# Kernel tuning notes

Hardware: AMD Instinct MI355X
Metric: run time of the kernel (lower is better)

## Reference

```python
import jax, jax.numpy as jnp
import numpy as np
from jax import lax

NUM_HEADS = 1
DN = ('NCHW', 'OIHW', 'NCHW')
EPS = 1e-12  # F.normalize default eps


def _l2_normalize(t):
    # F.normalize(t, dim=-1): t / max(||t||_2, eps)
    n = jnp.sqrt(jnp.sum(t * t, axis=-1, keepdims=True))
    return t / jnp.maximum(n, EPS)


def setup_inputs() -> dict:
    key = jax.random.key(0)
    k0, k1, k2, k3 = jax.random.split(key, 4)
    b, c, h, w = 4, 48, 256, 256
    x = jax.random.normal(k0, (b, c, h, w), dtype=jnp.float32)
    qkv_w = jax.random.normal(k1, (3 * c, c, 1, 1), dtype=jnp.float32) * 0.05
    dw_w = jax.random.normal(k2, (3 * c, 1, 3, 3), dtype=jnp.float32) * 0.05
    proj_w = jax.random.normal(k3, (c, c, 1, 1), dtype=jnp.float32) * 0.05
    temperature = jnp.ones((NUM_HEADS, 1, 1), dtype=jnp.float32)
    return {"x": x, "qkv_w": qkv_w, "dw_w": dw_w, "proj_w": proj_w,
            "temperature": temperature}


def reference(x, qkv_w, dw_w, proj_w, temperature):
    b, c, h, w = x.shape
    heads = NUM_HEADS
    # 1x1 conv to 3c channels, then 3x3 depthwise conv (groups = 3c)
    qkv = lax.conv_general_dilated(x, qkv_w, (1, 1), 'VALID', dimension_numbers=DN)
    qkv = lax.conv_general_dilated(qkv, dw_w, (1, 1), ((1, 1), (1, 1)),
                                   feature_group_count=3 * c, dimension_numbers=DN)
    q, k, v = jnp.split(qkv, 3, axis=1)
    # [b, heads, c_per_head, h*w]
    q = q.reshape(b, heads, c // heads, h * w)
    k = k.reshape(b, heads, c // heads, h * w)
    v = v.reshape(b, heads, c // heads, h * w)
    q = _l2_normalize(q)
    k = _l2_normalize(k)
    # channel-wise attention: [b, heads, c_per_head, c_per_head]
    attn = jax.nn.softmax(jnp.einsum('bhcn,bhdn->bhcd', q, k) * temperature, axis=-1)
    out = jnp.einsum('bhcd,bhdn->bhcn', attn, v).reshape(b, c, h, w)
    return lax.conv_general_dilated(out, proj_w, (1, 1), 'VALID', dimension_numbers=DN)
```

## Files before the change

### kernel.cpp

```cpp
#include <hip/hip_runtime.h>

#define B 4
#define C 48
#define C3 144
#define H 256
#define W 256
#define HW 65536
#define EPSN 1e-12f

#define TSX 16
#define TSY 12
#define HSX 18
#define HSY 14
#define NTX 16
#define NTY 22
#define NPIX2 192
#define NHALO 252

#define NCHUNK 128
#define CHUNK 512
#define LP 68

#define S_QKV_OFF  ((size_t)0)
#define S_DWQ_OFF  (S_QKV_OFF + (size_t)B * C3 * HW)
#define S_DWK_OFF  (S_DWQ_OFF + (size_t)B * C * HW)
#define S_SP_OFF   (S_DWK_OFF + (size_t)B * C * HW)
#define S_NQP_OFF  (S_SP_OFF + (size_t)B * NCHUNK * C * C)
#define S_NKP_OFF  (S_NQP_OFF + (size_t)B * NCHUNK * C)
#define S_S_OFF    (S_NKP_OFF + (size_t)B * NCHUNK * C)
#define S_NQ_OFF   (S_S_OFF + (size_t)B * C * C)
#define S_NK_OFF   (S_NQ_OFF + (size_t)B * C)
#define S_M_OFF    (S_NK_OFF + (size_t)B * C)
#define S_WT_OFF   (S_M_OFF + (size_t)B * C * C)
#define S_FLOATS   (S_WT_OFF + (size_t)C3 * C)

#define A_DWQ_OFF  ((size_t)0)
#define A_DWK_OFF  (A_DWQ_OFF + (size_t)B * C * HW)
#define A_SP_OFF   (A_DWK_OFF + (size_t)B * C * HW)
#define A_NQP_OFF  (A_SP_OFF + (size_t)B * NCHUNK * C * C)
#define A_NKP_OFF  (A_NQP_OFF + (size_t)B * NCHUNK * C)
#define A_S_OFF    (A_NKP_OFF + (size_t)B * NCHUNK * C)
#define A_NQ_OFF   (A_S_OFF + (size_t)B * C * C)
#define A_NK_OFF   (A_NQ_OFF + (size_t)B * C)
#define A_M_OFF    (A_NK_OFF + (size_t)B * C)
#define A_FLOATS   (A_M_OFF + (size_t)B * C * C)

#define B_S_OFF  0
#define B_NQ_OFF (B * C * C)
#define B_NK_OFF (B_NQ_OFF + B * C)
#define B_M_OFF  (B_NK_OFF + B * C)
#define B_ZERO_N (B * C * C + 2 * B * C)


__global__ __launch_bounds__(256) void s_wt(
    const float* __restrict__ w1, float* __restrict__ wT) {
  const int i = blockIdx.x * 256 + threadIdx.x;
  if (i < C3 * C) {
    const int oc = i / C, d = i - oc * C;
    wT[d * C3 + oc] = w1[i];
  }
}

__global__ __launch_bounds__(256) void s_conv1x1(
    const float* __restrict__ x, const float* __restrict__ wT,
    float* __restrict__ qkv) {
  __shared__ float xs[C * 256];
  const int t = threadIdx.x;
  const int bb = blockIdx.x >> 8;
  const int p0 = (blockIdx.x & 255) << 8;
  const float* xb = x + (size_t)bb * C * HW + p0;
#pragma unroll
  for (int j = 0; j < 12; ++j) {
    const int f = t + j * 256;
    const int d = f >> 6, p4 = (f & 63) * 4;
    *(float4*)&xs[d * 256 + p4] = *(const float4*)&xb[(size_t)d * HW + p4];
  }
  __syncthreads();
  const int pl = (t & 63) * 4;
  const int ocw = __builtin_amdgcn_readfirstlane((t >> 6) * 12);
#pragma unroll 1
  for (int g = 0; g < 3; ++g) {
    const int oc0 = g * 48 + ocw;
    const float* wp = wT + oc0;
    float acc[12][4];
#pragma unroll
    for (int o = 0; o < 12; ++o)
#pragma unroll
      for (int p = 0; p < 4; ++p) acc[o][p] = 0.f;
#pragma unroll 4
    for (int d = 0; d < C; ++d) {
      const float4 xv = *(const float4*)&xs[d * 256 + pl];
      const float xa[4] = {xv.x, xv.y, xv.z, xv.w};
#pragma unroll
      for (int jj = 0; jj < 3; ++jj) {
        const float4 wv = *(const float4*)&wp[d * C3 + jj * 4];
        const float wa[4] = {wv.x, wv.y, wv.z, wv.w};
#pragma unroll
        for (int o = 0; o < 4; ++o)
#pragma unroll
          for (int p = 0; p < 4; ++p)
            acc[jj * 4 + o][p] = fmaf(wa[o], xa[p], acc[jj * 4 + o][p]);
      }
    }
    float* ob = qkv + ((size_t)bb * C3 + oc0) * HW + p0 + pl;
#pragma unroll
    for (int o = 0; o < 12; ++o) {
      float4 v;
      v.x = acc[o][0]; v.y = acc[o][1]; v.z = acc[o][2]; v.w = acc[o][3];
      *(float4*)&ob[(size_t)o * HW] = v;
    }
  }
}

#define DWR 16
__global__ __launch_bounds__(256) void s_dw(
    const float* __restrict__ qkv, const float* __restrict__ w9,
    float* __restrict__ dwq, float* __restrict__ dwk,
    float* __restrict__ vout) {
  __shared__ float ls[18 * 260];
  const int t = threadIdx.x;
  const int rblk = blockIdx.x & 15;
  const int cb = blockIdx.x >> 4;
  const int c = cb % C3;
  const int bb = cb / C3;
  const int r0 = rblk * DWR;
  const float* src = qkv + (size_t)cb * HW;
#pragma unroll
  for (int f = t; f < 18 * 256; f += 256) {
    const int rr = f >> 8, xc = f & 255;
    const int gr = r0 - 1 + rr;
    ls[rr * 260 + 1 + xc] = (gr >= 0 && gr < H) ? src[gr * W + xc] : 0.f;
  }
  if (t < 18) { ls[t * 260] = 0.f; ls[t * 260 + 257] = 0.f; }
  const float* wp = w9 + c * 9;
  float wv[9];
#pragma unroll
  for (int k = 0; k < 9; ++k) wv[k] = wp[k];
  __syncthreads();
  float* dst;
  int cc;
  if (c < C)          { dst = dwq;  cc = c; }
  else if (c < 2 * C) { dst = dwk;  cc = c - C; }
  else                { dst = vout; cc = c - 2 * C; }
  float* ob = dst + ((size_t)bb * C + cc) * HW;
  const int xx = t;
#pragma unroll
  for (int ry = 0; ry < DWR; ++ry) {
    const float* l0 = ls + ry * 260 + xx;
    float d = wv[0] * l0[0] + wv[1] * l0[1] + wv[2] * l0[2];
    d = fmaf(wv[3], l0[260], d);
    d = fmaf(wv[4], l0[261], d);
    d = fmaf(wv[5], l0[262], d);
    d = fmaf(wv[6], l0[520], d);
    d = fmaf(wv[7], l0[521], d);
    d = fmaf(wv[8], l0[522], d);
    ob[(r0 + ry) * W + xx] = d;
  }
}


__global__ __launch_bounds__(256) void a1_conv_dw(
    const float* __restrict__ x, const float* __restrict__ w1,
    const float* __restrict__ w9, float* __restrict__ dwq,
    float* __restrict__ dwk, float* __restrict__ vout) {
  __shared__ float xs[C * 256];
  __shared__ float qs[8 * 256];
  __shared__ float wg[C * 8];
  __shared__ float wg9[8 * 9];
  const int t = threadIdx.x;
  const int bb = blockIdx.x / (NTX * NTY);
  const int tile = blockIdx.x % (NTX * NTY);
  const int ty = tile / NTX, tx = tile % NTX;

  const int hyy = t / HSX, hxx = t % HSX;
  const int hy = ty * TSY - 1 + hyy;
  const int hx = tx * TSX - 1 + hxx;
  const bool hin = (t < NHALO) && (hy >= 0) && (hy < H) && (hx >= 0) && (hx < W);
  const float* xb = x + (size_t)bb * C * HW + (hin ? (hy * W + hx) : 0);
#pragma unroll
  for (int ic = 0; ic < C; ++ic)
    xs[ic * 256 + t] = hin ? xb[(size_t)ic * HW] : 0.f;

  const int py = t / TSX, px = t % TSX;
  const int gy = ty * TSY + py, gx = tx * TSX + px;
  const bool pin = (t < NPIX2) && (gy < H);
  const int hpos = py * HSX + px;

  for (int grp = 0; grp < 18; ++grp) {
    const int ch0 = grp * 8;
    {
      const int j = t + ((t < 128) ? 256 : 0);
      if (t < 128) {
        const int ic = t >> 3, g = t & 7;
        wg[t] = w1[(ch0 + g) * C + ic];
        const int ic2 = j >> 3, g2 = j & 7;
        wg[j] = w1[(ch0 + g2) * C + ic2];
      } else if (t < 256) {
        const int r = t - 128;
        const int ic = (r + 128) >> 3, g = (r + 128) & 7;
        wg[r + 128] = w1[(ch0 + g) * C + ic];
      }
      if (t < 72) wg9[t] = w9[ch0 * 9 + t];
    }
    __syncthreads();

    float a[8];
#pragma unroll
    for (int g = 0; g < 8; ++g) a[g] = 0.f;
#pragma unroll 4
    for (int ic = 0; ic < C; ++ic) {
      const float xsv = xs[ic * 256 + t];
      const float4 w0 = *(const float4*)&wg[ic * 8];
      const float4 w4 = *(const float4*)&wg[ic * 8 + 4];
      a[0] = fmaf(w0.x, xsv, a[0]);
      a[1] = fmaf(w0.y, xsv, a[1]);
      a[2] = fmaf(w0.z, xsv, a[2]);
      a[3] = fmaf(w0.w, xsv, a[3]);
      a[4] = fmaf(w4.x, xsv, a[4]);
      a[5] = fmaf(w4.y, xsv, a[5]);
      a[6] = fmaf(w4.z, xsv, a[6]);
      a[7] = fmaf(w4.w, xsv, a[7]);
    }
#pragma unroll
    for (int g = 0; g < 8; ++g) qs[g * 256 + t] = a[g];
    __syncthreads();
    if (t < NPIX2) {
#pragma unroll
      for (int g = 0; g < 8; ++g) {
        const int ch = ch0 + g;
        const float* w9p = wg9 + g * 9;
        const float* q = qs + g * 256 + hpos;
        float d = w9p[0] * q[0] + w9p[1] * q[1] + w9p[2] * q[2];
        d = fmaf(w9p[3], q[HSX], d);
        d = fmaf(w9p[4], q[HSX + 1], d);
        d = fmaf(w9p[5], q[HSX + 2], d);
        d = fmaf(w9p[6], q[2 * HSX], d);
        d = fmaf(w9p[7], q[2 * HSX + 1], d);
        d = fmaf(w9p[8], q[2 * HSX + 2], d);
        if (pin) {
          float* dst;
          int cc;
          if (ch < C)          { dst = dwq; cc = ch; }
          else if (ch < 2 * C) { dst = dwk; cc = ch - C; }
          else                 { dst = vout; cc = ch - 2 * C; }
          dst[((size_t)bb * C + cc) * HW + gy * W + gx] = d;
        }
      }
    }
    __syncthreads();
  }
}

__global__ __launch_bounds__(256) void a2_gram(
    const float* __restrict__ dwq, const float* __restrict__ dwk,
    float* __restrict__ Sp, float* __restrict__ nqp, float* __restrict__ nkp) {
  __shared__ float qs[C * LP];
  __shared__ float ks[C * LP];
  const int tid = threadIdx.x;
  const int bb = blockIdx.x / NCHUNK;
  const int chunk = blockIdx.x % NCHUNK;
  const int base = chunk * CHUNK;
  const float* qb = dwq + (size_t)bb * C * HW + base;
  const float* kb = dwk + (size_t)bb * C * HW + base;
  const int c0 = (tid >> 4) * 3;
  const int d0 = (tid & 15) * 3;
  float acc[3][3] = {{0.f}};
  float nacc = 0.f;
  for (int sub = 0; sub < CHUNK / 64; ++sub) {
    __syncthreads();
#pragma unroll
    for (int j = 0; j < 3; ++j) {
      const int f = tid + j * 256;
      const int cc = f >> 4, p4 = (f & 15) * 4;
      *(float4*)&qs[cc * LP + p4] = *(const float4*)&qb[(size_t)cc * HW + sub * 64 + p4];
      *(float4*)&ks[cc * LP + p4] = *(const float4*)&kb[(size_t)cc * HW + sub * 64 + p4];
    }
    __syncthreads();
    if (tid < C) {
#pragma unroll
      for (int pp = 0; pp < 64; ++pp) { const float v = qs[tid * LP + pp]; nacc = fmaf(v, v, nacc); }
    } else if (tid >= 64 && tid < 64 + C) {
      const int c = tid - 64;
#pragma unroll
      for (int pp = 0; pp < 64; ++pp) { const float v = ks[c * LP + pp]; nacc = fmaf(v, v, nacc); }
    }
#pragma unroll 8
    for (int pp = 0; pp < 64; ++pp) {
      const float q0 = qs[(c0 + 0) * LP + pp];
      const float q1 = qs[(c0 + 1) * LP + pp];
      const float q2 = qs[(c0 + 2) * LP + pp];
      const float k0 = ks[(d0 + 0) * LP + pp];
      const float k1 = ks[(d0 + 1) * LP + pp];
      const float k2 = ks[(d0 + 2) * LP + pp];
      acc[0][0] = fmaf(q0, k0, acc[0][0]);
      acc[0][1] = fmaf(q0, k1, acc[0][1]);
      acc[0][2] = fmaf(q0, k2, acc[0][2]);
      acc[1][0] = fmaf(q1, k0, acc[1][0]);
      acc[1][1] = fmaf(q1, k1, acc[1][1]);
      acc[1][2] = fmaf(q1, k2, acc[1][2]);
      acc[2][0] = fmaf(q2, k0, acc[2][0]);
      acc[2][1] = fmaf(q2, k1, acc[2][1]);
      acc[2][2] = fmaf(q2, k2, acc[2][2]);
    }
  }
  float* Sb = Sp + ((size_t)bb * NCHUNK + chunk) * C * C;
#pragma unroll
  for (int i = 0; i < 3; ++i)
#pragma unroll
    for (int j = 0; j < 3; ++j)
      Sb[(c0 + i) * C + (d0 + j)] = acc[i][j];
  if (tid < C)                        nqp[((size_t)bb * NCHUNK + chunk) * C + tid] = nacc;
  else if (tid >= 64 && tid < 64 + C) nkp[((size_t)bb * NCHUNK + chunk) * C + (tid - 64)] = nacc;
}

#define RED_N (B * C * C + 2 * B * C)
__global__ __launch_bounds__(256) void a3a_reduce(
    const float* __restrict__ Sp, const float* __restrict__ nqp,
    const float* __restrict__ nkp, float* __restrict__ S,
    float* __restrict__ nq, float* __restrict__ nk) {
  const int gid = blockIdx.x * 256 + threadIdx.x;
  if (gid < B * C * C) {
    const int bb = gid / (C * C), j = gid - bb * (C * C);
    const float* src = Sp + (size_t)bb * NCHUNK * C * C + j;
    float s = 0.f;
#pragma unroll 8
    for (int i = 0; i < NCHUNK; ++i) s += src[(size_t)i * C * C];
    S[gid] = s;
  } else if (gid < B * C * C + B * C) {
    const int r = gid - B * C * C;
    const int bb = r / C, j = r - bb * C;
    const float* src = nqp + (size_t)bb * NCHUNK * C + j;
    float s = 0.f;
#pragma unroll 8
    for (int i = 0; i < NCHUNK; ++i) s += src[(size_t)i * C];
    nq[r] = s;
  } else if (gid < RED_N) {
    const int r = gid - B * C * C - B * C;
    const int bb = r / C, j = r - bb * C;
    const float* src = nkp + (size_t)bb * NCHUNK * C + j;
    float s = 0.f;
#pragma unroll 8
    for (int i = 0; i < NCHUNK; ++i) s += src[(size_t)i * C];
    nk[r] = s;
  }
}

__global__ __launch_bounds__(64) void a3b_attn(
    const float* __restrict__ S, const float* __restrict__ nq,
    const float* __restrict__ nk, const float* __restrict__ proj_w,
    const float* __restrict__ temperature, float* __restrict__ M) {
  __shared__ float A[C * C];
  __shared__ float knl[C];
  const int bb = blockIdx.x;
  const int t = threadIdx.x;
  const float T = temperature[0];
  if (t < C) knl[t] = fmaxf(sqrtf(nk[bb * C + t]), EPSN);
  __syncthreads();
  if (t < C) {
    const float qn = fmaxf(sqrtf(nq[bb * C + t]), EPSN);
    float row[C];
    float m = -1e30f;
    for (int d = 0; d < C; ++d) {
      const float v = S[(size_t)bb * C * C + t * C + d] / (qn * knl[d]) * T;
      row[d] = v;
      m = fmaxf(m, v);
    }
    float sum = 0.f;
    for (int d = 0; d < C; ++d) { const float e = expf(row[d] - m); row[d] = e; sum += e; }
    const float inv = 1.f / sum;
    for (int d = 0; d < C; ++d) A[t * C + d] = row[d] * inv;
  }
  __syncthreads();
  for (int idx = t; idx < C * C; idx += 64) {
    const int e = idx / C, d = idx % C;
    float acc = 0.f;
    for (int cc = 0; cc < C; ++cc) acc = fmaf(proj_w[e * C + cc], A[cc * C + d], acc);
    M[(size_t)bb * C * C + idx] = acc;
  }
}

__global__ __launch_bounds__(256) void a4_apply(
    float* __restrict__ out, const float* __restrict__ M) {
  __shared__ float vs[C * 64];
  __shared__ float Ms[C * C];
  const int t = threadIdx.x;
  const int bb = blockIdx.x >> 10;
  const int p0 = (blockIdx.x & 1023) << 6;
  float* ob = out + (size_t)bb * C * HW + p0;
#pragma unroll
  for (int j = 0; j < 3; ++j) {
    const int f = t + j * 256;
    const int d = f >> 4, p4 = (f & 15) * 4;
    *(float4*)&vs[d * 64 + p4] = *(const float4*)&ob[(size_t)d * HW + p4];
  }
  for (int j = t; j < C * C; j += 256) Ms[j] = M[bb * C * C + j];
  __syncthreads();
  const int pl = t & 63;
  const int e0 = (t >> 6) * 12;
  float acc[12];
#pragma unroll
  for (int j = 0; j < 12; ++j) acc[j] = 0.f;
  for (int d = 0; d < C; ++d) {
    const float vd = vs[d * 64 + pl];
#pragma unroll
    for (int j = 0; j < 12; ++j) acc[j] = fmaf(Ms[(e0 + j) * C + d], vd, acc[j]);
  }
#pragma unroll
  for (int j = 0; j < 12; ++j) ob[(size_t)(e0 + j) * HW + pl] = acc[j];
}


__global__ __launch_bounds__(256) void k0_zero(float* __restrict__ ws) {
  const int i = blockIdx.x * 256 + threadIdx.x;
  if (i < B_ZERO_N) ws[i] = 0.f;
}

#define TS 14
#define HS 16
#define NT 19
#define NPIX 196

__global__ __launch_bounds__(256) void k1_fused(
    const float* __restrict__ x, const float* __restrict__ w1,
    const float* __restrict__ w9, float* __restrict__ vout,
    float* __restrict__ S, float* __restrict__ nq, float* __restrict__ nk) {
  __shared__ float qs[4 * 256];
  __shared__ float qt[NPIX * C];
  __shared__ float kt[NPIX * C];
  const int t = threadIdx.x;
  const int bb = blockIdx.x / (NT * NT);
  const int tile = blockIdx.x % (NT * NT);
  const int ty = tile / NT, tx = tile % NT;
  const int hy = ty * TS - 1 + (t >> 4);
  const int hx = tx * TS - 1 + (t & 15);
  const bool hin = (hy >= 0 && hy < H && hx >= 0 && hx < W);
  const float* xb = x + (size_t)bb * C * HW;
  float xv[C];
#pragma unroll
  for (int ic = 0; ic < C; ++ic)
    xv[ic] = hin ? xb[(size_t)ic * HW + hy * W + hx] : 0.f;
  const int py = t / TS, px = t % TS;
  const int gy = ty * TS + py, gx = tx * TS + px;
  const bool pin = (t < NPIX) && (gy < H) && (gx < W);
  for (int grp = 0; grp < 36; ++grp) {
    const int ch0 = grp * 4;
    const float* wp = w1 + ch0 * C;
    float a0 = 0.f, a1 = 0.f, a2 = 0.f, a3 = 0.f;
#pragma unroll
    for (int ic = 0; ic < C; ++ic) {
      const float xs = xv[ic];
      a0 = fmaf(wp[ic], xs, a0);
      a1 = fmaf(wp[C + ic], xs, a1);
      a2 = fmaf(wp[2 * C + ic], xs, a2);
      a3 = fmaf(wp[3 * C + ic], xs, a3);
    }
    qs[0 * 256 + t] = a0;
    qs[1 * 256 + t] = a1;
    qs[2 * 256 + t] = a2;
    qs[3 * 256 + t] = a3;
    __syncthreads();
    if (t < NPIX) {
#pragma unroll
      for (int g = 0; g < 4; ++g) {
        const int ch = ch0 + g;
        const float* w9p = w9 + ch * 9;
        const float* q = qs + g * 256 + py * HS + px;
        float d = w9p[0] * q[0] + w9p[1] * q[1] + w9p[2] * q[2];
        d = fmaf(w9p[3], q[HS], d);
        d = fmaf(w9p[4], q[HS + 1], d);
        d = fmaf(w9p[5], q[HS + 2], d);
        d = fmaf(w9p[6], q[2 * HS], d);
        d = fmaf(w9p[7], q[2 * HS + 1], d);
        d = fmaf(w9p[8], q[2 * HS + 2], d);
        if (ch < C)          qt[t * C + ch] = pin ? d : 0.f;
        else if (ch < 2 * C) kt[t * C + (ch - C)] = pin ? d : 0.f;
        else if (pin)        vout[((size_t)bb * C + (ch - 2 * C)) * HW + gy * W + gx] = d;
      }
    }
    __syncthreads();
  }
  if (t < C) {
    float s = 0.f;
    for (int p = 0; p < NPIX; ++p) { const float v = qt[p * C + t]; s = fmaf(v, v, s); }
    atomicAdd(&nq[bb * C + t], s);
  } else if (t >= 64 && t < 64 + C) {
    const int c = t - 64;
    float s = 0.f;
    for (int p = 0; p < NPIX; ++p) { const float v = kt[p * C + c]; s = fmaf(v, v, s); }
    atomicAdd(&nk[bb * C + c], s);
  }
  {
    const int part = t >> 6;
    const int idx = t & 63;
    const int c0 = (idx >> 3) * 6;
    const int d0 = (idx & 7) * 6;
    float acc[6][6] = {{0.f}};
    const int p0 = part * 49;
    for (int p = p0; p < p0 + 49; ++p) {
      float qv[6], kv[6];
#pragma unroll
      for (int j = 0; j < 6; ++j) { qv[j] = qt[p * C + c0 + j]; kv[j] = kt[p * C + d0 + j]; }
#pragma unroll
      for (int i = 0; i < 6; ++i)
#pragma unroll
        for (int j = 0; j < 6; ++j) acc[i][j] = fmaf(qv[i], kv[j], acc[i][j]);
    }
    float* Sb = S + (size_t)bb * C * C;
#pragma unroll
    for (int i = 0; i < 6; ++i)
#pragma unroll
      for (int j = 0; j < 6; ++j) atomicAdd(&Sb[(c0 + i) * C + (d0 + j)], acc[i][j]);
  }
}


extern "C" void kernel_launch(void* const* d_in, const int* in_sizes, int n_in,
                              void* d_out, int out_size, void* d_ws, size_t ws_size,
                              hipStream_t stream) {
  const float* x      = (const float*)d_in[0];
  const float* qkv_w  = (const float*)d_in[1];
  const float* dw_w   = (const float*)d_in[2];
  const float* proj_w = (const float*)d_in[3];
  const float* temp   = (const float*)d_in[4];
  float* out = (float*)d_out;
  float* ws  = (float*)d_ws;

  if (ws_size >= S_FLOATS * sizeof(float)) {
    float* qkv = ws + S_QKV_OFF;
    float* dwq = ws + S_DWQ_OFF;
    float* dwk = ws + S_DWK_OFF;
    float* Sp  = ws + S_SP_OFF;
    float* nqp = ws + S_NQP_OFF;
    float* nkp = ws + S_NKP_OFF;
    float* S   = ws + S_S_OFF;
    float* nq  = ws + S_NQ_OFF;
    float* nk  = ws + S_NK_OFF;
    float* M   = ws + S_M_OFF;
    float* wT  = ws + S_WT_OFF;
    s_wt<<<(C3 * C + 255) / 256, 256, 0, stream>>>(qkv_w, wT);
    s_conv1x1<<<B * 256, 256, 0, stream>>>(x, wT, qkv);
    s_dw<<<B * C3 * 16, 256, 0, stream>>>(qkv, dw_w, dwq, dwk, out);
    a2_gram<<<B * NCHUNK, 256, 0, stream>>>(dwq, dwk, Sp, nqp, nkp);
    a3a_reduce<<<(RED_N + 255) / 256, 256, 0, stream>>>(Sp, nqp, nkp, S, nq, nk);
    a3b_attn<<<B, 64, 0, stream>>>(S, nq, nk, proj_w, temp, M);
    a4_apply<<<B * 1024, 256, 0, stream>>>(out, M);
  } else if (ws_size >= A_FLOATS * sizeof(float)) {
    float* dwq = ws + A_DWQ_OFF;
    float* dwk = ws + A_DWK_OFF;
    float* Sp  = ws + A_SP_OFF;
    float* nqp = ws + A_NQP_OFF;
    float* nkp = ws + A_NKP_OFF;
    float* S   = ws + A_S_OFF;
    float* nq  = ws + A_NQ_OFF;
    float* nk  = ws + A_NK_OFF;
    float* M   = ws + A_M_OFF;
    a1_conv_dw<<<B * NTX * NTY, 256, 0, stream>>>(x, qkv_w, dw_w, dwq, dwk, out);
    a2_gram<<<B * NCHUNK, 256, 0, stream>>>(dwq, dwk, Sp, nqp, nkp);
    a3a_reduce<<<(RED_N + 255) / 256, 256, 0, stream>>>(Sp, nqp, nkp, S, nq, nk);
    a3b_attn<<<B, 64, 0, stream>>>(S, nq, nk, proj_w, temp, M);
    a4_apply<<<B * 1024, 256, 0, stream>>>(out, M);
  } else {
    float* S  = ws + B_S_OFF;
    float* nq = ws + B_NQ_OFF;
    float* nk = ws + B_NK_OFF;
    float* M  = ws + B_M_OFF;
    k0_zero<<<(B_ZERO_N + 255) / 256, 256, 0, stream>>>(ws);
    k1_fused<<<B * NT * NT, 256, 0, stream>>>(x, qkv_w, dw_w, out, S, nq, nk);
    a3b_attn<<<B, 64, 0, stream>>>(S, nq, nk, proj_w, temp, M);
    a4_apply<<<B * 1024, 256, 0, stream>>>(out, M);
  }
}
```

Baseline: 345.0 us.

## Vectorize depthwise conv, gram and apply kernels with register tiling

Rewrites the depthwise conv so each thread computes four adjacent outputs from float4/float2 LDS reads and writes a float4. The gram kernel switches to float4 LDS loads for the dot products and norms. The apply kernel is restructured as a 4-pixel x 12-channel register tile per thread, reading a transposed mixing matrix straight from global memory (now written transposed by the attention kernel), with 4x fewer blocks. Weight offsets are forced into VGPRs instead of readfirstlane, which trades scalar loads for vector loads of the weights.

```diff
diff --git a/kernel.cpp b/kernel.cpp
--- a/kernel.cpp
+++ b/kernel.cpp
@@ -51,6 +51,11 @@
 #define B_M_OFF  (B_NK_OFF + B * C)
 #define B_ZERO_N (B * C * C + 2 * B * C)
 
+__device__ __forceinline__ int force_vgpr(int v) {
+  asm("v_mov_b32 %0, %1" : "=v"(v) : "v"(v));
+  return v;
+}
+
 
 __global__ __launch_bounds__(256) void s_wt(
     const float* __restrict__ w1, float* __restrict__ wT) {
@@ -77,7 +82,7 @@
   }
   __syncthreads();
   const int pl = (t & 63) * 4;
-  const int ocw = __builtin_amdgcn_readfirstlane((t >> 6) * 12);
+  const int ocw = force_vgpr((t >> 6) * 12);
 #pragma unroll 1
   for (int g = 0; g < 3; ++g) {
     const int oc0 = g * 48 + ocw;
@@ -143,18 +148,34 @@
   else if (c < 2 * C) { dst = dwk;  cc = c - C; }
   else                { dst = vout; cc = c - 2 * C; }
   float* ob = dst + ((size_t)bb * C + cc) * HW;
-  const int xx = t;
-#pragma unroll
-  for (int ry = 0; ry < DWR; ++ry) {
-    const float* l0 = ls + ry * 260 + xx;
-    float d = wv[0] * l0[0] + wv[1] * l0[1] + wv[2] * l0[2];
-    d = fmaf(wv[3], l0[260], d);
-    d = fmaf(wv[4], l0[261], d);
-    d = fmaf(wv[5], l0[262], d);
-    d = fmaf(wv[6], l0[520], d);
-    d = fmaf(wv[7], l0[521], d);
-    d = fmaf(wv[8], l0[522], d);
-    ob[(r0 + ry) * W + xx] = d;
+  const int xq = (t & 63) * 4;
+  const int rw = t >> 6;
+#pragma unroll
+  for (int rr = rw; rr < DWR; rr += 4) {
+    const float* l0 = ls + rr * 260 + xq;
+    const float4 a0 = *(const float4*)&l0[0];
+    const float2 b0 = *(const float2*)&l0[4];
+    const float4 a1 = *(const float4*)&l0[260];
+    const float2 b1 = *(const float2*)&l0[264];
+    const float4 a2 = *(const float4*)&l0[520];
+    const float2 b2 = *(const float2*)&l0[524];
+    const float r0e[6] = {a0.x, a0.y, a0.z, a0.w, b0.x, b0.y};
+    const float r1e[6] = {a1.x, a1.y, a1.z, a1.w, b1.x, b1.y};
+    const float r2e[6] = {a2.x, a2.y, a2.z, a2.w, b2.x, b2.y};
+    float4 o;
+    float* op = &o.x;
+#pragma unroll
+    for (int j = 0; j < 4; ++j) {
+      float d = wv[0] * r0e[j] + wv[1] * r0e[j + 1] + wv[2] * r0e[j + 2];
+      d = fmaf(wv[3], r1e[j], d);
+      d = fmaf(wv[4], r1e[j + 1], d);
+      d = fmaf(wv[5], r1e[j + 2], d);
+      d = fmaf(wv[6], r2e[j], d);
+      d = fmaf(wv[7], r2e[j + 1], d);
+      d = fmaf(wv[8], r2e[j + 2], d);
+      op[j] = d;
+    }
+    *(float4*)&ob[(r0 + rr) * W + xq] = o;
   }
 }
 
@@ -171,7 +192,6 @@
   const int bb = blockIdx.x / (NTX * NTY);
   const int tile = blockIdx.x % (NTX * NTY);
   const int ty = tile / NTX, tx = tile % NTX;
-
   const int hyy = t / HSX, hxx = t % HSX;
   const int hy = ty * TSY - 1 + hyy;
   const int hx = tx * TSX - 1 + hxx;
@@ -180,12 +200,10 @@
 #pragma unroll
   for (int ic = 0; ic < C; ++ic)
     xs[ic * 256 + t] = hin ? xb[(size_t)ic * HW] : 0.f;
-
   const int py = t / TSX, px = t % TSX;
   const int gy = ty * TSY + py, gx = tx * TSX + px;
   const bool pin = (t < NPIX2) && (gy < H);
   const int hpos = py * HSX + px;
-
   for (int grp = 0; grp < 18; ++grp) {
     const int ch0 = grp * 8;
     {
@@ -203,7 +221,6 @@
       if (t < 72) wg9[t] = w9[ch0 * 9 + t];
     }
     __syncthreads();
-
     float a[8];
 #pragma unroll
     for (int g = 0; g < 8; ++g) a[g] = 0.f;
@@ -278,29 +295,45 @@
     __syncthreads();
     if (tid < C) {
 #pragma unroll
-      for (int pp = 0; pp < 64; ++pp) { const float v = qs[tid * LP + pp]; nacc = fmaf(v, v, nacc); }
+      for (int pq = 0; pq < 64; pq += 4) {
+        const float4 v = *(const float4*)&qs[tid * LP + pq];
+        nacc = fmaf(v.x, v.x, nacc);
+        nacc = fmaf(v.y, v.y, nacc);
+        nacc = fmaf(v.z, v.z, nacc);
+        nacc = fmaf(v.w, v.w, nacc);
+      }
     } else if (tid >= 64 && tid < 64 + C) {
-      const int c = tid - 64;
-#pragma unroll
-      for (int pp = 0; pp < 64; ++pp) { const float v = ks[c * LP + pp]; nacc = fmaf(v, v, nacc); }
-    }
-#pragma unroll 8
-    for (int pp = 0; pp < 64; ++pp) {
-      const float q0 = qs[(c0 + 0) * LP + pp];
-      const float q1 = qs[(c0 + 1) * LP + pp];
-      const float q2 = qs[(c0 + 2) * LP + pp];
-      const float k0 = ks[(d0 + 0) * LP + pp];
-      const float k1 = ks[(d0 + 1) * LP + pp];
-      const float k2 = ks[(d0 + 2) * LP + pp];
-      acc[0][0] = fmaf(q0, k0, acc[0][0]);
-      acc[0][1] = fmaf(q0, k1, acc[0][1]);
-      acc[0][2] = fmaf(q0, k2, acc[0][2]);
-      acc[1][0] = fmaf(q1, k0, acc[1][0]);
-      acc[1][1] = fmaf(q1, k1, acc[1][1]);
-      acc[1][2] = fmaf(q1, k2, acc[1][2]);
-      acc[2][0] = fmaf(q2, k0, acc[2][0]);
-      acc[2][1] = fmaf(q2, k1, acc[2][1]);
-      acc[2][2] = fmaf(q2, k2, acc[2][2]);
+      const int cq = tid - 64;
+#pragma unroll
+      for (int pq = 0; pq < 64; pq += 4) {
+        const float4 v = *(const float4*)&ks[cq * LP + pq];
+        nacc = fmaf(v.x, v.x, nacc);
+        nacc = fmaf(v.y, v.y, nacc);
+        nacc = fmaf(v.z, v.z, nacc);
+        nacc = fmaf(v.w, v.w, nacc);
+      }
+    }
+#pragma unroll 4
+    for (int pq = 0; pq < 64; pq += 4) {
+      const float4 q0 = *(const float4*)&qs[(c0 + 0) * LP + pq];
+      const float4 q1 = *(const float4*)&qs[(c0 + 1) * LP + pq];
+      const float4 q2 = *(const float4*)&qs[(c0 + 2) * LP + pq];
+      const float4 k0 = *(const float4*)&ks[(d0 + 0) * LP + pq];
+      const float4 k1 = *(const float4*)&ks[(d0 + 1) * LP + pq];
+      const float4 k2 = *(const float4*)&ks[(d0 + 2) * LP + pq];
+      const float qa[3][4] = {{q0.x, q0.y, q0.z, q0.w},
+                              {q1.x, q1.y, q1.z, q1.w},
+                              {q2.x, q2.y, q2.z, q2.w}};
+      const float ka[3][4] = {{k0.x, k0.y, k0.z, k0.w},
+                              {k1.x, k1.y, k1.z, k1.w},
+                              {k2.x, k2.y, k2.z, k2.w}};
+#pragma unroll
+      for (int p = 0; p < 4; ++p)
+#pragma unroll
+        for (int i = 0; i < 3; ++i)
+#pragma unroll
+          for (int j = 0; j < 3; ++j)
+            acc[i][j] = fmaf(qa[i][p], ka[j][p], acc[i][j]);
     }
   }
   float* Sb = Sp + ((size_t)bb * NCHUNK + chunk) * C * C;
@@ -348,7 +381,7 @@
 __global__ __launch_bounds__(64) void a3b_attn(
     const float* __restrict__ S, const float* __restrict__ nq,
     const float* __restrict__ nk, const float* __restrict__ proj_w,
-    const float* __restrict__ temperature, float* __restrict__ M) {
+    const float* __restrict__ temperature, float* __restrict__ MT) {
   __shared__ float A[C * C];
   __shared__ float knl[C];
   const int bb = blockIdx.x;
@@ -375,38 +408,53 @@
     const int e = idx / C, d = idx % C;
     float acc = 0.f;
     for (int cc = 0; cc < C; ++cc) acc = fmaf(proj_w[e * C + cc], A[cc * C + d], acc);
-    M[(size_t)bb * C * C + idx] = acc;
+    MT[(size_t)bb * C * C + d * C + e] = acc;
   }
 }
 
 __global__ __launch_bounds__(256) void a4_apply(
-    float* __restrict__ out, const float* __restrict__ M) {
-  __shared__ float vs[C * 64];
-  __shared__ float Ms[C * C];
+    float* __restrict__ out, const float* __restrict__ MT) {
+  __shared__ float vs[C * 256];
   const int t = threadIdx.x;
-  const int bb = blockIdx.x >> 10;
-  const int p0 = (blockIdx.x & 1023) << 6;
+  const int bb = blockIdx.x >> 8;
+  const int p0 = (blockIdx.x & 255) << 8;
   float* ob = out + (size_t)bb * C * HW + p0;
 #pragma unroll
-  for (int j = 0; j < 3; ++j) {
+  for (int j = 0; j < 12; ++j) {
     const int f = t + j * 256;
-    const int d = f >> 4, p4 = (f & 15) * 4;
-    *(float4*)&vs[d * 64 + p4] = *(const float4*)&ob[(size_t)d * HW + p4];
-  }
-  for (int j = t; j < C * C; j += 256) Ms[j] = M[bb * C * C + j];
+    const int d = f >> 6, p4 = (f & 63) * 4;
+    *(float4*)&vs[d * 256 + p4] = *(const float4*)&ob[(size_t)d * HW + p4];
+  }
   __syncthreads();
-  const int pl = t & 63;
-  const int e0 = (t >> 6) * 12;
-  float acc[12];
-#pragma unroll
-  for (int j = 0; j < 12; ++j) acc[j] = 0.f;
+  const int pl = (t & 63) * 4;
+  const int e0 = force_vgpr((t >> 6) * 12);
+  const float* mb = MT + (size_t)bb * C * C + e0;
+  float acc[12][4];
+#pragma unroll
+  for (int o = 0; o < 12; ++o)
+#pragma unroll
+    for (int p = 0; p < 4; ++p) acc[o][p] = 0.f;
+#pragma unroll 4
   for (int d = 0; d < C; ++d) {
-    const float vd = vs[d * 64 + pl];
-#pragma unroll
-    for (int j = 0; j < 12; ++j) acc[j] = fmaf(Ms[(e0 + j) * C + d], vd, acc[j]);
-  }
-#pragma unroll
-  for (int j = 0; j < 12; ++j) ob[(size_t)(e0 + j) * HW + pl] = acc[j];
+    const float4 xv = *(const float4*)&vs[d * 256 + pl];
+    const float xa[4] = {xv.x, xv.y, xv.z, xv.w};
+#pragma unroll
+    for (int jj = 0; jj < 3; ++jj) {
+      const float4 wv = *(const float4*)&mb[d * C + jj * 4];
+      const float wa[4] = {wv.x, wv.y, wv.z, wv.w};
+#pragma unroll
+      for (int o = 0; o < 4; ++o)
+#pragma unroll
+        for (int p = 0; p < 4; ++p)
+          acc[jj * 4 + o][p] = fmaf(wa[o], xa[p], acc[jj * 4 + o][p]);
+    }
+  }
+#pragma unroll
+  for (int o = 0; o < 12; ++o) {
+    float4 v;
+    v.x = acc[o][0]; v.y = acc[o][1]; v.z = acc[o][2]; v.w = acc[o][3];
+    *(float4*)&ob[(size_t)(e0 + o) * HW + pl] = v;
+  }
 }
 
 
@@ -535,15 +583,15 @@
     float* S   = ws + S_S_OFF;
     float* nq  = ws + S_NQ_OFF;
     float* nk  = ws + S_NK_OFF;
-    float* M   = ws + S_M_OFF;
+    float* MT  = ws + S_M_OFF;
     float* wT  = ws + S_WT_OFF;
     s_wt<<<(C3 * C + 255) / 256, 256, 0, stream>>>(qkv_w, wT);
     s_conv1x1<<<B * 256, 256, 0, stream>>>(x, wT, qkv);
     s_dw<<<B * C3 * 16, 256, 0, stream>>>(qkv, dw_w, dwq, dwk, out);
     a2_gram<<<B * NCHUNK, 256, 0, stream>>>(dwq, dwk, Sp, nqp, nkp);
     a3a_reduce<<<(RED_N + 255) / 256, 256, 0, stream>>>(Sp, nqp, nkp, S, nq, nk);
-    a3b_attn<<<B, 64, 0, stream>>>(S, nq, nk, proj_w, temp, M);
-    a4_apply<<<B * 1024, 256, 0, stream>>>(out, M);
+    a3b_attn<<<B, 64, 0, stream>>>(S, nq, nk, proj_w, temp, MT);
+    a4_apply<<<B * 256, 256, 0, stream>>>(out, MT);
   } else if (ws_size >= A_FLOATS * sizeof(float)) {
     float* dwq = ws + A_DWQ_OFF;
     float* dwk = ws + A_DWK_OFF;
@@ -553,20 +601,20 @@
     float* S   = ws + A_S_OFF;
     float* nq  = ws + A_NQ_OFF;
     float* nk  = ws + A_NK_OFF;
-    float* M   = ws + A_M_OFF;
+    float* MT  = ws + A_M_OFF;
     a1_conv_dw<<<B * NTX * NTY, 256, 0, stream>>>(x, qkv_w, dw_w, dwq, dwk, out);
     a2_gram<<<B * NCHUNK, 256, 0, stream>>>(dwq, dwk, Sp, nqp, nkp);
     a3a_reduce<<<(RED_N + 255) / 256, 256, 0, stream>>>(Sp, nqp, nkp, S, nq, nk);
-    a3b_attn<<<B, 64, 0, stream>>>(S, nq, nk, proj_w, temp, M);
-    a4_apply<<<B * 1024, 256, 0, stream>>>(out, M);
+    a3b_attn<<<B, 64, 0, stream>>>(S, nq, nk, proj_w, temp, MT);
+    a4_apply<<<B * 256, 256, 0, stream>>>(out, MT);
   } else {
     float* S  = ws + B_S_OFF;
     float* nq = ws + B_NQ_OFF;
     float* nk = ws + B_NK_OFF;
-    float* M  = ws + B_M_OFF;
+    float* MT = ws + B_M_OFF;
     k0_zero<<<(B_ZERO_N + 255) / 256, 256, 0, stream>>>(ws);
     k1_fused<<<B * NT * NT, 256, 0, stream>>>(x, qkv_w, dw_w, out, S, nq, nk);
-    a3b_attn<<<B, 64, 0, stream>>>(S, nq, nk, proj_w, temp, M);
-    a4_apply<<<B * 1024, 256, 0, stream>>>(out, M);
-  }
-}
+    a3b_attn<<<B, 64, 0, stream>>>(S, nq, nk, proj_w, temp, MT);
+    a4_apply<<<B * 256, 256, 0, stream>>>(out, MT);
+  }
+}
```

Measured after the change: 346.6 us. Within noise of the previous version (+0.5%).
